# Kernel optimization log

Measured on AMD Instinct MI355X. Metric: run time of the kernel, lower is better.

Reference implementation:

```python
import jax, jax.numpy as jnp
import numpy as np

E1, E2, E3, M, DEC_H, OUT = 512, 512, 512, 1024, 2048, 1000
B = 16384

def _linear_params(key, fan_in, fan_out):
    kw, kb = jax.random.split(key)
    bound = 1.0 / np.sqrt(fan_in)
    W = jax.random.uniform(kw, (fan_out, fan_in), jnp.float32, -bound, bound)
    b = jax.random.uniform(kb, (fan_out,), jnp.float32, -bound, bound)
    return W, b

def setup_inputs() -> dict:
    key = jax.random.key(0)
    ks = jax.random.split(key, 7)
    tube = jax.random.normal(ks[0], (B, E1 + E2 + E3), jnp.float32)
    w1_W, w1_b = _linear_params(ks[1], E1, M)
    w2_W, w2_b = _linear_params(ks[2], E2, M)
    w3_W, w3_b = _linear_params(ks[3], E3, M)
    wh_W, wh_b = _linear_params(ks[4], 3 * M, M)
    wd1_W, wd1_b = _linear_params(ks[5], 2 * M, DEC_H)
    wd2_W, wd2_b = _linear_params(ks[6], DEC_H, OUT)
    return dict(tube=tube, w1_W=w1_W, w1_b=w1_b, w2_W=w2_W, w2_b=w2_b,
                w3_W=w3_W, w3_b=w3_b, wh_W=wh_W, wh_b=wh_b,
                wd1_W=wd1_W, wd1_b=wd1_b, wd2_W=wd2_W, wd2_b=wd2_b)

def reference(tube, w1_W, w1_b, w2_W, w2_b, w3_W, w3_b, wh_W, wh_b,
              wd1_W, wd1_b, wd2_W, wd2_b):
    relu = jax.nn.relu
    x1 = tube[:, :E1]
    x2 = tube[:, E1:E1 + E2]
    x3 = tube[:, E1 + E2:E1 + E2 + E3]
    P1 = relu(x1 @ w1_W.T + w1_b)   # [B, M]
    P2 = relu(x2 @ w2_W.T + w2_b)
    P3 = relu(x3 @ w3_W.T + w3_b)
    hid1 = jnp.concatenate([P1, P2, P3], axis=1)      # [B, 3M]
    last_hid = relu(hid1 @ wh_W.T + wh_b)             # [B, M]
    # diag(matmul(last_hid, P.T)) == row-wise dot product
    alpha1 = jnp.sum(last_hid * P1, axis=1)
    alpha2 = jnp.sum(last_hid * P2, axis=1)
    alpha3 = jnp.sum(last_hid * P3, axis=1)
    alphas = jnp.stack([alpha1, alpha2, alpha3], axis=1)  # [B, 3]
    weights = jax.nn.softmax(alphas, axis=1)
    context = (weights[:, 0:1] * P1 + weights[:, 1:2] * P2
               + weights[:, 2:3] * P3)                   # [B, M]
    decode_start = jnp.concatenate([context, last_hid], axis=1)  # [B, 2M]
    out = relu(decode_start @ wd1_W.T + wd1_b)
    out = out @ wd2_W.T + wd2_b                           # [B, OUT]
    return out
```

## Files before the change

### kernel.cpp

```cpp
#include <hip/hip_runtime.h>
#include <hip/hip_bf16.h>


typedef __bf16 bf16_t;
typedef __bf16 bf16x4 __attribute__((ext_vector_type(4)));
typedef __bf16 bf16x8 __attribute__((ext_vector_type(8)));
typedef float  f32x4  __attribute__((ext_vector_type(4)));

#define AS1(p) (const __attribute__((address_space(1))) void*)(p)
#define AS3(p) (__attribute__((address_space(3))) void*)(p)

__global__ void cvt_f32_bf16_v4(const float* __restrict__ src, bf16_t* __restrict__ dst,
                                int n4src, int n4tot) {
  for (int i = blockIdx.x * blockDim.x + threadIdx.x; i < n4tot; i += gridDim.x * blockDim.x) {
    bf16x4 o;
    if (i < n4src) {
      float4 f = ((const float4*)src)[i];
      o[0] = (bf16_t)f.x; o[1] = (bf16_t)f.y; o[2] = (bf16_t)f.z; o[3] = (bf16_t)f.w;
    } else {
      o[0] = (bf16_t)0.0f; o[1] = (bf16_t)0.0f; o[2] = (bf16_t)0.0f; o[3] = (bf16_t)0.0f;
    }
    *(bf16x4*)(dst + (size_t)i * 4) = o;
  }
}

__global__ void concat_bias3(const float* __restrict__ a, const float* __restrict__ b,
                             const float* __restrict__ c, float* __restrict__ dst) {
  int i = blockIdx.x * blockDim.x + threadIdx.x;
  if (i < 1024) dst[i] = a[i];
  else if (i < 2048) dst[i] = b[i - 1024];
  else if (i < 3072) dst[i] = c[i - 2048];
}

template<bool BDIAG, bool RELU, bool OUT_BF16>
__global__ __launch_bounds__(512, 2)
void gemm256(const bf16_t* __restrict__ A, int lda,
             const bf16_t* __restrict__ Bw, int ldb,
             const float* __restrict__ bias,
             void* __restrict__ Cout, int ldc,
             int K, int Nmask, int nbx)
{
  extern __shared__ char lds[];
  bf16_t* Ab = (bf16_t*)lds;
  bf16_t* Bb = (bf16_t*)(lds + 65536);

  const int t   = threadIdx.x;
  const int ln  = t & 63;
  const int w   = t >> 6;
  const int l15 = ln & 15, lhi = ln >> 4;
  const int wm  = w >> 2, wn = w & 3;

  const int nb = (int)gridDim.x;
  const int id = (int)blockIdx.x;
  const int id_sw = (id & 7) * (nb >> 3) + (id >> 3);
  const int bx = id_sw % nbx, by = id_sw / nbx;
  const int rowBase = by * 256;
  const int colBase = bx * 256;
  const int aCol0 = BDIAG ? (colBase >> 10) * 512 : 0;

  const int srow = (w << 4) + (ln >> 2);
  const int scol = (((ln & 3) ^ (ln >> 3)) & 3) << 3;

  const bf16_t* aS = A  + (size_t)(rowBase + srow) * lda + aCol0 + scol;
  const bf16_t* bS = Bw + (size_t)(colBase + srow) * ldb + scol;
  const size_t aI = (size_t)128 * lda;
  const size_t bI = (size_t)128 * ldb;
  bf16_t* daW = Ab + (w << 9);
  bf16_t* dbW = Bb + (w << 9);

  const int key  = (l15 >> 1) & 3;
  const int fcol = (lhi ^ key) << 3;
  const int aOff = (wm * 128 + l15) * 32 + fcol;
  const int bOff = (wn * 64  + l15) * 32 + fcol;

  const int nt = K >> 5;

  f32x4 acc[8][4] = {};

  #define STAGE(kt, s)                                                              \
    do {                                                                            \
      const bf16_t* a_ = aS + (size_t)(kt) * 32;                                    \
      const bf16_t* b_ = bS + (size_t)(kt) * 32;                                    \
      bf16_t* da_ = daW + (s) * 8192;                                               \
      bf16_t* db_ = dbW + (s) * 8192;                                               \
      __builtin_amdgcn_global_load_lds(AS1(a_),      AS3(da_),        16, 0, 0);    \
      __builtin_amdgcn_global_load_lds(AS1(a_ + aI), AS3(da_ + 4096), 16, 0, 0);    \
      __builtin_amdgcn_global_load_lds(AS1(b_),      AS3(db_),        16, 0, 0);    \
      __builtin_amdgcn_global_load_lds(AS1(b_ + bI), AS3(db_ + 4096), 16, 0, 0);    \
    } while (0)

  STAGE(0, 0); STAGE(1, 1); STAGE(2, 2);
  asm volatile("s_waitcnt vmcnt(8)" ::: "memory");
  __builtin_amdgcn_s_barrier();
  asm volatile("" ::: "memory");

  for (int j = 0; j < nt; ++j) {
    const int s = j & 3;
    const bf16_t* As_ = Ab + s * 8192 + aOff;
    const bf16_t* Bs_ = Bb + s * 8192 + bOff;

    bf16x8 af[8], bfr[4];
    af[0] = *(const bf16x8*)(As_);
    af[1] = *(const bf16x8*)(As_ + 512);
    #pragma unroll
    for (int nf = 0; nf < 4; ++nf)
      bfr[nf] = *(const bf16x8*)(Bs_ + nf * 512);

    if (j + 3 < nt) STAGE(j + 3, ((j + 3) & 3));

    #pragma unroll
    for (int mf = 2; mf < 8; ++mf)
      af[mf] = *(const bf16x8*)(As_ + mf * 512);

    __builtin_amdgcn_s_setprio(1);
    #pragma unroll
    for (int mf = 0; mf < 8; ++mf)
      #pragma unroll
      for (int nf = 0; nf < 4; ++nf)
        acc[mf][nf] = __builtin_amdgcn_mfma_f32_16x16x32_bf16(af[mf], bfr[nf], acc[mf][nf], 0, 0, 0);
    __builtin_amdgcn_s_setprio(0);

    if (j + 3 < nt) {
      asm volatile("s_waitcnt vmcnt(8)" ::: "memory");
    } else if (j + 2 < nt) {
      asm volatile("s_waitcnt vmcnt(4)" ::: "memory");
    } else if (j + 1 < nt) {
      asm volatile("s_waitcnt vmcnt(0)" ::: "memory");
    }
    asm volatile("s_waitcnt lgkmcnt(0)" ::: "memory");
    __builtin_amdgcn_s_barrier();
    asm volatile("" ::: "memory");
  }
  #undef STAGE

  #pragma unroll
  for (int mf = 0; mf < 8; ++mf) {
    const int row = rowBase + wm * 128 + mf * 16 + lhi * 4;
    #pragma unroll
    for (int nf = 0; nf < 4; ++nf) {
      const int col = colBase + wn * 64 + nf * 16 + l15;
      const float bv = (col < Nmask) ? bias[col] : 0.0f;
      #pragma unroll
      for (int i = 0; i < 4; ++i) {
        float v = acc[mf][nf][i] + bv;
        if (RELU) v = fmaxf(v, 0.0f);
        if (OUT_BF16) {
          ((bf16_t*)Cout)[(size_t)(row + i) * ldc + col] = (bf16_t)v;
        } else {
          if (col < Nmask) ((float*)Cout)[(size_t)(row + i) * ldc + col] = v;
        }
      }
    }
  }
}

__global__ __launch_bounds__(256)
void attn_ctx(const bf16_t* __restrict__ P, bf16_t* __restrict__ ds) {
  __shared__ float red[3][4];
  __shared__ float wsh[3];
  const int r = blockIdx.x;
  const int t = threadIdx.x;
  const bf16_t* Prow = P + (size_t)r * 3072;
  bf16_t* dsrow = ds + (size_t)r * 2048;

  const int j = t * 4;
  bf16x4 lv = *(const bf16x4*)(dsrow + 1024 + j);
  float lhv[4], pv[3][4];
  float s[3] = {0.f, 0.f, 0.f};
  #pragma unroll
  for (int q = 0; q < 4; q++) lhv[q] = (float)lv[q];
  #pragma unroll
  for (int e = 0; e < 3; e++) {
    bf16x4 p = *(const bf16x4*)(Prow + e * 1024 + j);
    #pragma unroll
    for (int q = 0; q < 4; q++) {
      pv[e][q] = (float)p[q];
      s[e] += lhv[q] * pv[e][q];
    }
  }
  #pragma unroll
  for (int off = 32; off > 0; off >>= 1) {
    #pragma unroll
    for (int e = 0; e < 3; e++) s[e] += __shfl_down(s[e], off, 64);
  }
  const int w = t >> 6, l = t & 63;
  if (l == 0) {
    #pragma unroll
    for (int e = 0; e < 3; e++) red[e][w] = s[e];
  }
  __syncthreads();
  if (t == 0) {
    float a0 = red[0][0] + red[0][1] + red[0][2] + red[0][3];
    float a1 = red[1][0] + red[1][1] + red[1][2] + red[1][3];
    float a2 = red[2][0] + red[2][1] + red[2][2] + red[2][3];
    float mx = fmaxf(a0, fmaxf(a1, a2));
    float e0 = expf(a0 - mx), e1 = expf(a1 - mx), e2 = expf(a2 - mx);
    float inv = 1.0f / (e0 + e1 + e2);
    wsh[0] = e0 * inv; wsh[1] = e1 * inv; wsh[2] = e2 * inv;
  }
  __syncthreads();
  const float w0 = wsh[0], w1 = wsh[1], w2 = wsh[2];
  bf16x4 o;
  #pragma unroll
  for (int q = 0; q < 4; q++)
    o[q] = (bf16_t)(w0 * pv[0][q] + w1 * pv[1][q] + w2 * pv[2][q]);
  *(bf16x4*)(dsrow + j) = o;
}

extern "C" void kernel_launch(void* const* d_in, const int* in_sizes, int n_in,
                              void* d_out, int out_size, void* d_ws, size_t ws_size,
                              hipStream_t stream) {
  (void)in_sizes; (void)n_in; (void)out_size; (void)ws_size;

  const float* tube = (const float*)d_in[0];
  const float* w1W  = (const float*)d_in[1];
  const float* w1b  = (const float*)d_in[2];
  const float* w2W  = (const float*)d_in[3];
  const float* w2b  = (const float*)d_in[4];
  const float* w3W  = (const float*)d_in[5];
  const float* w3b  = (const float*)d_in[6];
  const float* whW  = (const float*)d_in[7];
  const float* whb  = (const float*)d_in[8];
  const float* wd1W = (const float*)d_in[9];
  const float* wd1b = (const float*)d_in[10];
  const float* wd2W = (const float*)d_in[11];
  const float* wd2b = (const float*)d_in[12];

  char* ws = (char*)d_ws;
  bf16_t* P       = (bf16_t*)(ws + 0);
  bf16_t* ds      = (bf16_t*)(ws + 100663296);
  bf16_t* wd1B    = (bf16_t*)(ws + 167772160);
  bf16_t* wd2B    = (bf16_t*)(ws + 176160768);
  bf16_t* whB     = (bf16_t*)(ws + 180355072);
  bf16_t* w123B   = (bf16_t*)(ws + 186646528);
  bf16_t* tubeB   = (bf16_t*)(ws + 189792256);
  bf16_t* out1    = (bf16_t*)(ws + 180355072);
  float*  bias123 = (float*)(ws + 247463936);

  hipFuncSetAttribute((const void*)(gemm256<true,  true,  true >),
                      hipFuncAttributeMaxDynamicSharedMemorySize, 131072);
  hipFuncSetAttribute((const void*)(gemm256<false, true,  true >),
                      hipFuncAttributeMaxDynamicSharedMemorySize, 131072);
  hipFuncSetAttribute((const void*)(gemm256<false, false, false>),
                      hipFuncAttributeMaxDynamicSharedMemorySize, 131072);

  auto cvt = [&](const float* s, bf16_t* d, int n4s, int n4t) {
    int nb = (n4t + 255) / 256; if (nb > 2048) nb = 2048;
    hipLaunchKernelGGL(cvt_f32_bf16_v4, dim3(nb), dim3(256), 0, stream, s, d, n4s, n4t);
  };
  cvt(tube, tubeB, 6291456, 6291456);
  cvt(w1W,  w123B,           131072, 131072);
  cvt(w2W,  w123B +  524288, 131072, 131072);
  cvt(w3W,  w123B + 1048576, 131072, 131072);
  cvt(whW,  whB,  786432, 786432);
  cvt(wd1W, wd1B, 1048576, 1048576);
  cvt(wd2W, wd2B, 512000, 524288);
  hipLaunchKernelGGL(concat_bias3, dim3(12), dim3(256), 0, stream, w1b, w2b, w3b, bias123);

  hipLaunchKernelGGL((gemm256<true, true, true>), dim3(12 * 64), dim3(512), 131072, stream,
                     tubeB, 1536, w123B, 512, bias123, (void*)P, 3072, 512, 3072, 12);
  hipLaunchKernelGGL((gemm256<false, true, true>), dim3(4 * 64), dim3(512), 131072, stream,
                     P, 3072, whB, 3072, whb, (void*)(ds + 1024), 2048, 3072, 1024, 4);
  hipLaunchKernelGGL(attn_ctx, dim3(16384), dim3(256), 0, stream, P, ds);
  hipLaunchKernelGGL((gemm256<false, true, true>), dim3(8 * 64), dim3(512), 131072, stream,
                     ds, 2048, wd1B, 2048, wd1b, (void*)out1, 2048, 2048, 2048, 8);
  hipLaunchKernelGGL((gemm256<false, false, false>), dim3(4 * 64), dim3(512), 131072, stream,
                     out1, 2048, wd2B, 2048, wd2b, d_out, 1000, 2048, 1000, 4);
}
```

Before: 440.1 us.

## Move GEMM barrier before MFMA loop and fuse weight conversion kernels

The GEMM main loop now loads all A/B fragments from LDS, issues the next prefetch stage, then waits and barriers before running the MFMAs, instead of barriering after the MFMA block. This changes how LDS reads, global-to-LDS prefetch and compute overlap, and may shorten the critical path or serialize it further. Separately, the six per-weight conversion launches are merged into one grid-stride kernel to cut launch overhead.

```diff
diff --git a/kernel.cpp b/kernel.cpp
--- a/kernel.cpp
+++ b/kernel.cpp
@@ -21,6 +21,31 @@
       o[0] = (bf16_t)0.0f; o[1] = (bf16_t)0.0f; o[2] = (bf16_t)0.0f; o[3] = (bf16_t)0.0f;
     }
     *(bf16x4*)(dst + (size_t)i * 4) = o;
+  }
+}
+
+__global__ void cvt_weights(const float* __restrict__ w1, const float* __restrict__ w2,
+                            const float* __restrict__ w3, const float* __restrict__ wh,
+                            const float* __restrict__ wd1, const float* __restrict__ wd2,
+                            bf16_t* __restrict__ w123, bf16_t* __restrict__ whB,
+                            bf16_t* __restrict__ wd1B, bf16_t* __restrict__ wd2B) {
+  const int stride = gridDim.x * blockDim.x;
+  for (int i = blockIdx.x * blockDim.x + threadIdx.x; i < 2752512; i += stride) {
+    const float* s; bf16_t* d; int o; int ns = 1 << 30;
+    if (i < 131072)       { s = w1;  d = w123;           o = i; }
+    else if (i < 262144)  { s = w2;  d = w123 + 524288;  o = i - 131072; }
+    else if (i < 393216)  { s = w3;  d = w123 + 1048576; o = i - 262144; }
+    else if (i < 1179648) { s = wh;  d = whB;            o = i - 393216; }
+    else if (i < 2228224) { s = wd1; d = wd1B;           o = i - 1179648; }
+    else                  { s = wd2; d = wd2B;           o = i - 2228224; ns = 512000; }
+    bf16x4 v;
+    if (o < ns) {
+      float4 f = ((const float4*)s)[o];
+      v[0] = (bf16_t)f.x; v[1] = (bf16_t)f.y; v[2] = (bf16_t)f.z; v[3] = (bf16_t)f.w;
+    } else {
+      v[0] = (bf16_t)0.0f; v[1] = (bf16_t)0.0f; v[2] = (bf16_t)0.0f; v[3] = (bf16_t)0.0f;
+    }
+    *(bf16x4*)(d + (size_t)o * 4) = v;
   }
 }
 
@@ -100,17 +125,22 @@
     const bf16_t* Bs_ = Bb + s * 8192 + bOff;
 
     bf16x8 af[8], bfr[4];
-    af[0] = *(const bf16x8*)(As_);
-    af[1] = *(const bf16x8*)(As_ + 512);
-    #pragma unroll
-    for (int nf = 0; nf < 4; ++nf)
-      bfr[nf] = *(const bf16x8*)(Bs_ + nf * 512);
-
-    if (j + 3 < nt) STAGE(j + 3, ((j + 3) & 3));
-
-    #pragma unroll
-    for (int mf = 2; mf < 8; ++mf)
-      af[mf] = *(const bf16x8*)(As_ + mf * 512);
+    #pragma unroll
+    for (int mf = 0; mf < 8; ++mf) af[mf] = *(const bf16x8*)(As_ + mf * 512);
+    #pragma unroll
+    for (int nf = 0; nf < 4; ++nf) bfr[nf] = *(const bf16x8*)(Bs_ + nf * 512);
+
+    if (j + 3 < nt) {
+      STAGE(j + 3, ((j + 3) & 3));
+      asm volatile("s_waitcnt vmcnt(8)" ::: "memory");
+    } else if (j + 2 < nt) {
+      asm volatile("s_waitcnt vmcnt(4)" ::: "memory");
+    } else if (j + 1 < nt) {
+      asm volatile("s_waitcnt vmcnt(0)" ::: "memory");
+    }
+    asm volatile("s_waitcnt lgkmcnt(0)" ::: "memory");
+    __builtin_amdgcn_s_barrier();
+    asm volatile("" ::: "memory");
 
     __builtin_amdgcn_s_setprio(1);
     #pragma unroll
@@ -119,17 +149,6 @@
       for (int nf = 0; nf < 4; ++nf)
         acc[mf][nf] = __builtin_amdgcn_mfma_f32_16x16x32_bf16(af[mf], bfr[nf], acc[mf][nf], 0, 0, 0);
     __builtin_amdgcn_s_setprio(0);
-
-    if (j + 3 < nt) {
-      asm volatile("s_waitcnt vmcnt(8)" ::: "memory");
-    } else if (j + 2 < nt) {
-      asm volatile("s_waitcnt vmcnt(4)" ::: "memory");
-    } else if (j + 1 < nt) {
-      asm volatile("s_waitcnt vmcnt(0)" ::: "memory");
-    }
-    asm volatile("s_waitcnt lgkmcnt(0)" ::: "memory");
-    __builtin_amdgcn_s_barrier();
-    asm volatile("" ::: "memory");
   }
   #undef STAGE
 
@@ -244,17 +263,10 @@
   hipFuncSetAttribute((const void*)(gemm256<false, false, false>),
                       hipFuncAttributeMaxDynamicSharedMemorySize, 131072);
 
-  auto cvt = [&](const float* s, bf16_t* d, int n4s, int n4t) {
-    int nb = (n4t + 255) / 256; if (nb > 2048) nb = 2048;
-    hipLaunchKernelGGL(cvt_f32_bf16_v4, dim3(nb), dim3(256), 0, stream, s, d, n4s, n4t);
-  };
-  cvt(tube, tubeB, 6291456, 6291456);
-  cvt(w1W,  w123B,           131072, 131072);
-  cvt(w2W,  w123B +  524288, 131072, 131072);
-  cvt(w3W,  w123B + 1048576, 131072, 131072);
-  cvt(whW,  whB,  786432, 786432);
-  cvt(wd1W, wd1B, 1048576, 1048576);
-  cvt(wd2W, wd2B, 512000, 524288);
+  hipLaunchKernelGGL(cvt_f32_bf16_v4, dim3(2048), dim3(256), 0, stream,
+                     tube, tubeB, 6291456, 6291456);
+  hipLaunchKernelGGL(cvt_weights, dim3(2048), dim3(256), 0, stream,
+                     w1W, w2W, w3W, whW, wd1W, wd2W, w123B, whB, wd1B, wd2B);
   hipLaunchKernelGGL(concat_bias3, dim3(12), dim3(256), 0, stream, w1b, w2b, w3b, bias123);
 
   hipLaunchKernelGGL((gemm256<true, true, true>), dim3(12 * 64), dim3(512), 131072, stream,
```

New measurement: 416.7 us. 1.06x faster.
